# Optimization experiments

Measured on AMD Instinct MI355X. Metric: run time of the kernel, lower is better.

Reference implementation:

```python
import jax, jax.numpy as jnp
import numpy as np

B, S, D = 32, 576, 768
G = 24  # sqrt(S)
TEMP = 0.01


def grid_sample_bilinear_zeros(img, grid):
    # img: (B,C,H,W), grid: (B,Hg,Wg,2) in [-1,1]; torch F.grid_sample,
    # mode='bilinear', padding_mode='zeros', align_corners=False
    Bn, C, H, W = img.shape
    gx, gy = grid[..., 0], grid[..., 1]
    ix = ((gx + 1.0) * W - 1.0) * 0.5
    iy = ((gy + 1.0) * H - 1.0) * 0.5
    x0 = jnp.floor(ix); y0 = jnp.floor(iy)
    x1 = x0 + 1.0;      y1 = y0 + 1.0
    wx1 = ix - x0; wx0 = 1.0 - wx1
    wy1 = iy - y0; wy0 = 1.0 - wy1

    def gather(xi, yi):
        valid = (xi >= 0) & (xi <= W - 1) & (yi >= 0) & (yi <= H - 1)
        xc = jnp.clip(xi, 0, W - 1).astype(jnp.int32)
        yc = jnp.clip(yi, 0, H - 1).astype(jnp.int32)
        vals = jax.vmap(lambda im, y, x: im[:, y, x])(img, yc, xc)  # (B,C,Hg,Wg)
        return vals * valid.astype(img.dtype)[:, None, :, :]

    return (gather(x0, y0) * (wx0 * wy0)[:, None]
            + gather(x1, y0) * (wx1 * wy0)[:, None]
            + gather(x0, y1) * (wx0 * wy1)[:, None]
            + gather(x1, y1) * (wx1 * wy1)[:, None])


def key_finder_net(h, W1, b1, W2, b2, W3, b3):
    # fc1 -> relu -> fc2 -> relu -> fc3 -> tanh
    h = jax.nn.relu(h @ W1 + b1)
    h = jax.nn.relu(h @ W2 + b2)
    return jnp.tanh(h @ W3 + b3)


def setup_inputs() -> dict:
    key = jax.random.key(0)
    ks = jax.random.split(key, 16)
    sd = 1.0 / np.sqrt(D)
    inp = {
        'x': jax.random.normal(ks[0], (B, S, D), dtype=jnp.float32),
        'indices': jax.random.randint(ks[1], (B, S), 0, S),
        'Wq': jax.random.normal(ks[2], (D, D), dtype=jnp.float32) * sd,
        'bq': jnp.zeros((D,), jnp.float32),
        'Wk': jax.random.normal(ks[3], (D, D), dtype=jnp.float32) * sd,
        'bk': jnp.zeros((D,), jnp.float32),
        'Wv': jax.random.normal(ks[4], (D, D), dtype=jnp.float32) * sd,
        'bv': jnp.zeros((D,), jnp.float32),
        'W1': jax.random.normal(ks[5], (2 * D, 60), dtype=jnp.float32) / np.sqrt(2 * D),
        'b1': jnp.zeros((60,), jnp.float32),
        'W2': jax.random.normal(ks[6], (60, 60), dtype=jnp.float32) / np.sqrt(60),
        'b2': jnp.zeros((60,), jnp.float32),
        'W3': jax.random.normal(ks[7], (60, 2), dtype=jnp.float32) / np.sqrt(60),
        'b3': jnp.zeros((2,), jnp.float32),
    }
    return inp


def reference(x, indices, Wq, bq, Wk, bk, Wv, bv, W1, b1, W2, b2, W3, b3):
    q = x @ Wq + bq  # (B,S,D)
    k = x @ Wk + bk
    v = x @ Wv + bv

    sample = key_finder_net(jnp.concatenate([q, k], axis=2), W1, b1, W2, b2, W3, b3)  # (B,S,2)
    # torch: cat((sample_x, sample_y), dim=1).reshape(B,G,G,2)
    flat = jnp.concatenate([sample[:, :, 0], sample[:, :, 1]], axis=1)  # (B,2S)
    grid = flat.reshape(B, G, G, 2)

    k_img = jnp.transpose(k, (0, 2, 1)).reshape(B, D, G, G)
    v_img = jnp.transpose(v, (0, 2, 1)).reshape(B, D, G, G)

    sk = grid_sample_bilinear_zeros(k_img, grid)  # (B,D,G,G)
    sv = grid_sample_bilinear_zeros(v_img, grid)
    sampled_key = jnp.transpose(sk.reshape(B, D, G * G), (0, 2, 1))   # (B,S,D)
    sampled_value = jnp.transpose(sv.reshape(B, D, G * G), (0, 2, 1))

    scores = jnp.sum(q * sampled_key, axis=-1)  # (B,S)
    return jax.nn.sigmoid(TEMP * scores)[..., None] * sampled_value
```

## Files before the change

### kernel.cpp

```cpp
#include <hip/hip_runtime.h>

typedef _Float16 f16;
typedef _Float16 f16x8 __attribute__((ext_vector_type(8)));
typedef _Float16 f16x4 __attribute__((ext_vector_type(4)));
typedef float f32x4 __attribute__((ext_vector_type(4)));

constexpr int NB = 32, NS = 576, ND = 768, NG = 24;
constexpr int M_TOT = NB * NS;
constexpr int N_TOT = 3 * ND;

__global__ void cast_x_kernel(const float* __restrict__ x, f16* __restrict__ xb) {
  int i = (blockIdx.x * 256 + threadIdx.x) * 4;
  float4 v = *(const float4*)(x + i);
  f16x4 o;
  o.x = (f16)v.x; o.y = (f16)v.y; o.z = (f16)v.z; o.w = (f16)v.w;
  *(f16x4*)(xb + i) = o;
}

__global__ __launch_bounds__(256) void cast_w_t_kernel(const float* __restrict__ Wq,
                                                       const float* __restrict__ Wk,
                                                       const float* __restrict__ Wv,
                                                       f16* __restrict__ WT) {
  __shared__ float tile[64][65];
  int bt = blockIdx.x;
  int ntile = bt / 12, ktile = bt % 12;
  const float* src = (ntile < 12) ? Wq : ((ntile < 24) ? Wk : Wv);
  int n0 = (ntile % 12) * 64, k0 = ktile * 64;
  int cc = threadIdx.x & 63, rr = threadIdx.x >> 6;
#pragma unroll
  for (int i = 0; i < 16; i++) {
    int k = rr + i * 4;
    tile[cc][k] = src[(size_t)(k0 + k) * ND + n0 + cc];
  }
  __syncthreads();
#pragma unroll
  for (int i = 0; i < 16; i++) {
    int n = rr + i * 4;
    WT[(size_t)(ntile * 64 + n) * ND + k0 + cc] = (f16)tile[n][cc];
  }
}

__global__ __launch_bounds__(256) void wcT_kernel(const float* __restrict__ Wq,
                                                  const float* __restrict__ Wk,
                                                  const float* __restrict__ bq,
                                                  const float* __restrict__ bk,
                                                  const float* __restrict__ W1,
                                                  const float* __restrict__ b1,
                                                  f16* __restrict__ WcT_hi,
                                                  f16* __restrict__ WcT_lo,
                                                  float* __restrict__ bc) {
  if (blockIdx.x == 768) {
    int c = threadIdx.x;
    if (c < 60) {
      float acc = b1[c];
      for (int j = 0; j < ND; j++)
        acc += bq[j] * W1[j * 60 + c] + bk[j] * W1[(ND + j) * 60 + c];
      bc[c] = acc;
    }
    return;
  }
  __shared__ float part[4][64];
  int r = blockIdx.x;
  int wave = threadIdx.x >> 6, lane = threadIdx.x & 63;
  int c = (lane < 60) ? lane : 59;
  const float* wq = Wq + (size_t)r * ND;
  const float* wk = Wk + (size_t)r * ND;
  float acc = 0.f;
  int j0 = wave * 192;
  for (int j = j0; j < j0 + 192; j++)
    acc += wq[j] * W1[j * 60 + c] + wk[j] * W1[(ND + j) * 60 + c];
  part[wave][lane] = acc;
  __syncthreads();
  if (wave == 0 && lane < 60) {
    float v = part[0][lane] + part[1][lane] + part[2][lane] + part[3][lane];
    f16 hi = (f16)v;
    WcT_hi[(size_t)lane * ND + r] = hi;
    WcT_lo[(size_t)lane * ND + r] = (f16)(v - (float)hi);
  }
}

__device__ __forceinline__ void async_copy16(const f16* g, f16* l) {
  __builtin_amdgcn_global_load_lds((const __attribute__((address_space(1))) void*)g,
                                   (__attribute__((address_space(3))) void*)l, 16, 0, 0);
}

__global__ __launch_bounds__(256) void gemm_kernel(const f16* __restrict__ A,
                                                   const f16* __restrict__ Bt,
                                                   const float* __restrict__ bq,
                                                   const float* __restrict__ bk,
                                                   const float* __restrict__ bv,
                                                   f16* __restrict__ C) {
  constexpr int BM = 128, BK = 64;
  __shared__ __align__(16) f16 sA[BM * BK];
  __shared__ __align__(16) f16 sB[BM * BK];

  int bm = blockIdx.x % (M_TOT / BM);
  int bn = blockIdx.x / (M_TOT / BM);
  int tid = threadIdx.x;
  int wave = tid >> 6, lane = tid & 63;
  int wm = (wave >> 1) * 64, wn = (wave & 1) * 64;
  int m0 = bm * BM, n0 = bn * BM;

  int srow = tid >> 3;
  int gchunk = ((tid & 7) ^ (srow & 7)) * 8;

  f32x4 acc[4][4];
#pragma unroll
  for (int i = 0; i < 4; i++)
#pragma unroll
    for (int j = 0; j < 4; j++) acc[i][j] = 0.f;

  int q = lane >> 4, r16 = lane & 15;

  for (int kk = 0; kk < ND; kk += BK) {
#pragma unroll
    for (int ps = 0; ps < 4; ps++) {
      async_copy16(A + (size_t)(m0 + ps * 32 + srow) * ND + kk + gchunk, sA + ps * 2048 + tid * 8);
      async_copy16(Bt + (size_t)(n0 + ps * 32 + srow) * ND + kk + gchunk, sB + ps * 2048 + tid * 8);
    }
    __syncthreads();

#pragma unroll
    for (int h = 0; h < 2; h++) {
      f16x8 aF[4], bF[4];
#pragma unroll
      for (int mt = 0; mt < 4; mt++) {
        int R = wm + mt * 16 + r16;
        aF[mt] = *(const f16x8*)(sA + R * 64 + (((h * 4 + q) ^ (R & 7)) * 8));
      }
#pragma unroll
      for (int nt = 0; nt < 4; nt++) {
        int R = wn + nt * 16 + r16;
        bF[nt] = *(const f16x8*)(sB + R * 64 + (((h * 4 + q) ^ (R & 7)) * 8));
      }
#pragma unroll
      for (int mt = 0; mt < 4; mt++)
#pragma unroll
        for (int nt = 0; nt < 4; nt++)
          acc[mt][nt] = __builtin_amdgcn_mfma_f32_16x16x32_f16(bF[nt], aF[mt], acc[mt][nt], 0, 0, 0);
    }
    __syncthreads();
  }

#pragma unroll
  for (int mt = 0; mt < 4; mt++) {
    int gm = m0 + wm + mt * 16 + r16;
#pragma unroll
    for (int nt = 0; nt < 4; nt++) {
      int gn0 = n0 + wn + nt * 16 + q * 4;
      const float* bp = (gn0 < ND) ? (bq + gn0)
                      : ((gn0 < 2 * ND) ? (bk + gn0 - ND) : (bv + gn0 - 2 * ND));
      float4 bias = *(const float4*)bp;
      f16x4 o;
      o[0] = (f16)(acc[mt][nt][0] + bias.x);
      o[1] = (f16)(acc[mt][nt][1] + bias.y);
      o[2] = (f16)(acc[mt][nt][2] + bias.z);
      o[3] = (f16)(acc[mt][nt][3] + bias.w);
      *(f16x4*)(C + (size_t)gm * N_TOT + gn0) = o;
    }
  }
}

__global__ __launch_bounds__(256) void z1_mfma_kernel(const float* __restrict__ x,
                                                      const f16* __restrict__ WcT_hi,
                                                      const f16* __restrict__ WcT_lo,
                                                      const float* __restrict__ bc,
                                                      float* __restrict__ h1) {
  __shared__ float red[3][16][64];
  int wave = threadIdx.x >> 6, lane = threadIdx.x & 63;
  int q = lane >> 4, r16 = lane & 15;
  int m0 = blockIdx.x * 16;
  int k0 = wave * 192;
  const float* xr = x + (size_t)(m0 + r16) * ND + k0;

  f32x4 acc[4];
#pragma unroll
  for (int nf = 0; nf < 4; nf++) acc[nf] = 0.f;

  for (int kk = 0; kk < 192; kk += 32) {
    int ko = kk + q * 8;
    float4 v0 = *(const float4*)(xr + ko);
    float4 v1 = *(const float4*)(xr + ko + 4);
    f16x8 a_hi, a_lo;
    float xv[8] = {v0.x, v0.y, v0.z, v0.w, v1.x, v1.y, v1.z, v1.w};
#pragma unroll
    for (int j = 0; j < 8; j++) {
      f16 h = (f16)xv[j];
      a_hi[j] = h;
      a_lo[j] = (f16)(xv[j] - (float)h);
    }
    f16x8 b_hi[4], b_lo[4];
#pragma unroll
    for (int nf = 0; nf < 4; nf++) {
      size_t off = (size_t)(nf * 16 + r16) * ND + k0 + ko;
      b_hi[nf] = *(const f16x8*)(WcT_hi + off);
      b_lo[nf] = *(const f16x8*)(WcT_lo + off);
    }
#pragma unroll
    for (int nf = 0; nf < 4; nf++) {
      acc[nf] = __builtin_amdgcn_mfma_f32_16x16x32_f16(a_hi, b_hi[nf], acc[nf], 0, 0, 0);
      acc[nf] = __builtin_amdgcn_mfma_f32_16x16x32_f16(a_lo, b_hi[nf], acc[nf], 0, 0, 0);
      acc[nf] = __builtin_amdgcn_mfma_f32_16x16x32_f16(a_hi, b_lo[nf], acc[nf], 0, 0, 0);
    }
  }

  if (wave > 0) {
#pragma unroll
    for (int nf = 0; nf < 4; nf++)
#pragma unroll
      for (int r = 0; r < 4; r++) red[wave - 1][nf * 4 + r][lane] = acc[nf][r];
  }
  __syncthreads();
  if (wave == 0) {
#pragma unroll
    for (int nf = 0; nf < 4; nf++) {
      int col = nf * 16 + r16;
      if (col < 60) {
        float bcv = bc[col];
#pragma unroll
        for (int r = 0; r < 4; r++) {
          float v = acc[nf][r] + red[0][nf * 4 + r][lane] + red[1][nf * 4 + r][lane]
                  + red[2][nf * 4 + r][lane] + bcv;
          h1[(size_t)(m0 + q * 4 + r) * 60 + col] = fmaxf(v, 0.f);
        }
      }
    }
  }
}

__global__ void mlp_tail_kernel(const float* __restrict__ h1, const float* __restrict__ W2,
                                const float* __restrict__ b2, const float* __restrict__ W3,
                                const float* __restrict__ b3, float* __restrict__ coords) {
  int m = (blockIdx.x * 256 + threadIdx.x) >> 6;
  int lane = threadIdx.x & 63;
  int cl = (lane < 60) ? lane : 59;
  const float* h = h1 + (size_t)m * 60;
  float acc = b2[cl];
  for (int j = 0; j < 60; j++) acc = fmaf(h[j], W2[j * 60 + cl], acc);
  float h2 = fmaxf(acc, 0.f);
  float p0 = (lane < 60) ? h2 * W3[cl * 2 + 0] : 0.f;
  float p1 = (lane < 60) ? h2 * W3[cl * 2 + 1] : 0.f;
#pragma unroll
  for (int o = 32; o > 0; o >>= 1) { p0 += __shfl_down(p0, o); p1 += __shfl_down(p1, o); }
  if (lane == 0) {
    float s0 = tanhf(p0 + b3[0]);
    float s1 = tanhf(p1 + b3[1]);
    int b = m / NS, s = m % NS;
    float* cb = coords + (size_t)b * (2 * NS);
    cb[(s >> 1) * 2 + (s & 1)] = s0;
    cb[(288 + (s >> 1)) * 2 + (s & 1)] = s1;
  }
}

__global__ __launch_bounds__(256) void sample_kernel(const f16* __restrict__ qkv,
                                                     const float* __restrict__ coords,
                                                     float* __restrict__ out) {
  int wave = threadIdx.x >> 6, t = threadIdx.x & 63;
  int idx = blockIdx.x * 4 + wave;
  int b = idx / NS, p = idx % NS;

  float gx = coords[(size_t)b * (2 * NS) + p * 2 + 0];
  float gy = coords[(size_t)b * (2 * NS) + p * 2 + 1];
  float ix = ((gx + 1.f) * (float)NG - 1.f) * 0.5f;
  float iy = ((gy + 1.f) * (float)NG - 1.f) * 0.5f;
  float x0f = floorf(ix), y0f = floorf(iy);
  float wx1 = ix - x0f, wx0 = 1.f - wx1;
  float wy1 = iy - y0f, wy0 = 1.f - wy1;
  int x0 = (int)x0f, y0 = (int)y0f, x1 = x0 + 1, y1 = y0 + 1;
  bool vx0 = (x0 >= 0) & (x0 <= NG - 1), vx1 = (x1 >= 0) & (x1 <= NG - 1);
  bool vy0 = (y0 >= 0) & (y0 <= NG - 1), vy1 = (y1 >= 0) & (y1 <= NG - 1);
  int cx0 = min(max(x0, 0), NG - 1), cx1 = min(max(x1, 0), NG - 1);
  int cy0 = min(max(y0, 0), NG - 1), cy1 = min(max(y1, 0), NG - 1);
  float w00 = wx0 * wy0 * ((vx0 && vy0) ? 1.f : 0.f);
  float w10 = wx1 * wy0 * ((vx1 && vy0) ? 1.f : 0.f);
  float w01 = wx0 * wy1 * ((vx0 && vy1) ? 1.f : 0.f);
  float w11 = wx1 * wy1 * ((vx1 && vy1) ? 1.f : 0.f);

  size_t base = (size_t)b * NS;
  const f16* r00 = qkv + (base + cy0 * NG + cx0) * N_TOT;
  const f16* r10 = qkv + (base + cy0 * NG + cx1) * N_TOT;
  const f16* r01 = qkv + (base + cy1 * NG + cx0) * N_TOT;
  const f16* r11 = qkv + (base + cy1 * NG + cx1) * N_TOT;
  const f16* qr  = qkv + (base + p) * N_TOT;

  int d0 = t * 12;
  float partial = 0.f;
  float outv[12];
#pragma unroll
  for (int ch = 0; ch < 3; ch++) {
    int d = d0 + ch * 4;
    f16x4 k00 = *(const f16x4*)(r00 + ND + d);
    f16x4 k10 = *(const f16x4*)(r10 + ND + d);
    f16x4 k01 = *(const f16x4*)(r01 + ND + d);
    f16x4 k11 = *(const f16x4*)(r11 + ND + d);
    f16x4 v00 = *(const f16x4*)(r00 + 2 * ND + d);
    f16x4 v10 = *(const f16x4*)(r10 + 2 * ND + d);
    f16x4 v01 = *(const f16x4*)(r01 + 2 * ND + d);
    f16x4 v11 = *(const f16x4*)(r11 + 2 * ND + d);
    f16x4 qv  = *(const f16x4*)(qr + d);
#pragma unroll
    for (int j = 0; j < 4; j++) {
      float sk = w00 * (float)k00[j] + w10 * (float)k10[j]
               + w01 * (float)k01[j] + w11 * (float)k11[j];
      float sv = w00 * (float)v00[j] + w10 * (float)v10[j]
               + w01 * (float)v01[j] + w11 * (float)v11[j];
      partial = fmaf((float)qv[j], sk, partial);
      outv[ch * 4 + j] = sv;
    }
  }
#pragma unroll
  for (int o = 32; o > 0; o >>= 1) partial += __shfl_down(partial, o);
  float score = __shfl(partial, 0);
  float sig = 1.f / (1.f + expf(-0.01f * score));
  float* orow = out + (size_t)(base + p) * ND;
#pragma unroll
  for (int ch = 0; ch < 3; ch++) {
    float4 st;
    st.x = sig * outv[ch * 4 + 0]; st.y = sig * outv[ch * 4 + 1];
    st.z = sig * outv[ch * 4 + 2]; st.w = sig * outv[ch * 4 + 3];
    *(float4*)(orow + d0 + ch * 4) = st;
  }
}

extern "C" void kernel_launch(void* const* d_in, const int* in_sizes, int n_in,
                              void* d_out, int out_size, void* d_ws, size_t ws_size,
                              hipStream_t stream) {
  const float* x  = (const float*)d_in[0];
  const float* Wq = (const float*)d_in[2];
  const float* bq = (const float*)d_in[3];
  const float* Wk = (const float*)d_in[4];
  const float* bk = (const float*)d_in[5];
  const float* Wv = (const float*)d_in[6];
  const float* bv = (const float*)d_in[7];
  const float* W1 = (const float*)d_in[8];
  const float* b1 = (const float*)d_in[9];
  const float* W2 = (const float*)d_in[10];
  const float* b2 = (const float*)d_in[11];
  const float* W3 = (const float*)d_in[12];
  const float* b3 = (const float*)d_in[13];
  float* out = (float*)d_out;

  char* ws = (char*)d_ws;
  f16*   xb     = (f16*)(ws);
  f16*   WT     = (f16*)(ws + 28311552);
  f16*   qkv    = (f16*)(ws + 31850496);
  f16*   WcT_hi = (f16*)(ws + 31850496);
  f16*   WcT_lo = (f16*)(ws + 31948800);
  float* bc     = (float*)(ws + 116969472);
  float* h1     = (float*)(ws + 116969728);
  float* coords = (float*)(ws + 121393408);

  cast_x_kernel<<<dim3(M_TOT * ND / 1024), dim3(256), 0, stream>>>(x, xb);
  cast_w_t_kernel<<<dim3(432), dim3(256), 0, stream>>>(Wq, Wk, Wv, WT);
  wcT_kernel<<<dim3(769), dim3(256), 0, stream>>>(Wq, Wk, bq, bk, W1, b1, WcT_hi, WcT_lo, bc);
  z1_mfma_kernel<<<dim3(M_TOT / 16), dim3(256), 0, stream>>>(x, WcT_hi, WcT_lo, bc, h1);
  gemm_kernel<<<dim3((M_TOT / 128) * (N_TOT / 128)), dim3(256), 0, stream>>>(xb, WT, bq, bk, bv, qkv);
  mlp_tail_kernel<<<dim3(M_TOT / 4), dim3(256), 0, stream>>>(h1, W2, b2, W3, b3, coords);
  sample_kernel<<<dim3(M_TOT / 4), dim3(256), 0, stream>>>(qkv, coords, out);
  (void)in_sizes; (void)n_in; (void)out_size; (void)ws_size;
}
```

Baseline: 355.6 us.

## Fuse x cast and MLP tail into the first-layer MFMA kernel

```diff
diff --git a/kernel.cpp b/kernel.cpp
--- a/kernel.cpp
+++ b/kernel.cpp
@@ -8,14 +8,6 @@
 constexpr int NB = 32, NS = 576, ND = 768, NG = 24;
 constexpr int M_TOT = NB * NS;
 constexpr int N_TOT = 3 * ND;
-
-__global__ void cast_x_kernel(const float* __restrict__ x, f16* __restrict__ xb) {
-  int i = (blockIdx.x * 256 + threadIdx.x) * 4;
-  float4 v = *(const float4*)(x + i);
-  f16x4 o;
-  o.x = (f16)v.x; o.y = (f16)v.y; o.z = (f16)v.z; o.w = (f16)v.w;
-  *(f16x4*)(xb + i) = o;
-}
 
 __global__ __launch_bounds__(256) void cast_w_t_kernel(const float* __restrict__ Wq,
                                                        const float* __restrict__ Wk,
@@ -79,6 +71,106 @@
   }
 }
 
+__global__ __launch_bounds__(256) void z1_fused_kernel(const float* __restrict__ x,
+                                                       const f16* __restrict__ WcT_hi,
+                                                       const f16* __restrict__ WcT_lo,
+                                                       const float* __restrict__ bc,
+                                                       const float* __restrict__ W2,
+                                                       const float* __restrict__ b2,
+                                                       const float* __restrict__ W3,
+                                                       const float* __restrict__ b3,
+                                                       f16* __restrict__ xb,
+                                                       float* __restrict__ coords) {
+  __shared__ float red[3][16][64];
+  __shared__ float htile[16][60];
+  int wave = threadIdx.x >> 6, lane = threadIdx.x & 63;
+  int q = lane >> 4, r16 = lane & 15;
+  int m0 = blockIdx.x * 16;
+  int k0 = wave * 192;
+  const float* xr = x + (size_t)(m0 + r16) * ND + k0;
+  f16* xbr = xb + (size_t)(m0 + r16) * ND + k0;
+
+  f32x4 acc[4];
+#pragma unroll
+  for (int nf = 0; nf < 4; nf++) acc[nf] = 0.f;
+
+  for (int kk = 0; kk < 192; kk += 32) {
+    int ko = kk + q * 8;
+    float4 v0 = *(const float4*)(xr + ko);
+    float4 v1 = *(const float4*)(xr + ko + 4);
+    f16x8 a_hi, a_lo;
+    float xv[8] = {v0.x, v0.y, v0.z, v0.w, v1.x, v1.y, v1.z, v1.w};
+#pragma unroll
+    for (int j = 0; j < 8; j++) {
+      f16 h = (f16)xv[j];
+      a_hi[j] = h;
+      a_lo[j] = (f16)(xv[j] - (float)h);
+    }
+    *(f16x8*)(xbr + ko) = a_hi;
+    f16x8 b_hi[4], b_lo[4];
+#pragma unroll
+    for (int nf = 0; nf < 4; nf++) {
+      size_t off = (size_t)(nf * 16 + r16) * ND + k0 + ko;
+      b_hi[nf] = *(const f16x8*)(WcT_hi + off);
+      b_lo[nf] = *(const f16x8*)(WcT_lo + off);
+    }
+#pragma unroll
+    for (int nf = 0; nf < 4; nf++) {
+      acc[nf] = __builtin_amdgcn_mfma_f32_16x16x32_f16(a_hi, b_hi[nf], acc[nf], 0, 0, 0);
+      acc[nf] = __builtin_amdgcn_mfma_f32_16x16x32_f16(a_lo, b_hi[nf], acc[nf], 0, 0, 0);
+      acc[nf] = __builtin_amdgcn_mfma_f32_16x16x32_f16(a_hi, b_lo[nf], acc[nf], 0, 0, 0);
+    }
+  }
+
+  if (wave > 0) {
+#pragma unroll
+    for (int nf = 0; nf < 4; nf++)
+#pragma unroll
+      for (int r = 0; r < 4; r++) red[wave - 1][nf * 4 + r][lane] = acc[nf][r];
+  }
+  __syncthreads();
+  if (wave == 0) {
+#pragma unroll
+    for (int nf = 0; nf < 4; nf++) {
+      int col = nf * 16 + r16;
+      if (col < 60) {
+        float bcv = bc[col];
+#pragma unroll
+        for (int r = 0; r < 4; r++) {
+          float v = acc[nf][r] + red[0][nf * 4 + r][lane] + red[1][nf * 4 + r][lane]
+                  + red[2][nf * 4 + r][lane] + bcv;
+          htile[q * 4 + r][col] = fmaxf(v, 0.f);
+        }
+      }
+    }
+  }
+  __syncthreads();
+
+  int c = (lane < 60) ? lane : 59;
+  float b2v = b2[c];
+  float w30 = W3[c * 2 + 0], w31 = W3[c * 2 + 1];
+#pragma unroll
+  for (int rr = 0; rr < 4; rr++) {
+    int row = wave * 4 + rr;
+    float acc2 = b2v;
+    for (int j = 0; j < 60; j++) acc2 = fmaf(htile[row][j], W2[j * 60 + c], acc2);
+    float h2 = fmaxf(acc2, 0.f);
+    float p0 = (lane < 60) ? h2 * w30 : 0.f;
+    float p1 = (lane < 60) ? h2 * w31 : 0.f;
+#pragma unroll
+    for (int o = 32; o > 0; o >>= 1) { p0 += __shfl_down(p0, o); p1 += __shfl_down(p1, o); }
+    if (lane == 0) {
+      float s0 = tanhf(p0 + b3[0]);
+      float s1 = tanhf(p1 + b3[1]);
+      int m = m0 + row;
+      int b = m / NS, s = m % NS;
+      float* cb = coords + (size_t)b * (2 * NS);
+      cb[(s >> 1) * 2 + (s & 1)] = s0;
+      cb[(288 + (s >> 1)) * 2 + (s & 1)] = s1;
+    }
+  }
+}
+
 __device__ __forceinline__ void async_copy16(const f16* g, f16* l) {
   __builtin_amdgcn_global_load_lds((const __attribute__((address_space(1))) void*)g,
                                    (__attribute__((address_space(3))) void*)l, 16, 0, 0);
@@ -158,97 +250,6 @@
       o[3] = (f16)(acc[mt][nt][3] + bias.w);
       *(f16x4*)(C + (size_t)gm * N_TOT + gn0) = o;
     }
-  }
-}
-
-__global__ __launch_bounds__(256) void z1_mfma_kernel(const float* __restrict__ x,
-                                                      const f16* __restrict__ WcT_hi,
-                                                      const f16* __restrict__ WcT_lo,
-                                                      const float* __restrict__ bc,
-                                                      float* __restrict__ h1) {
-  __shared__ float red[3][16][64];
-  int wave = threadIdx.x >> 6, lane = threadIdx.x & 63;
-  int q = lane >> 4, r16 = lane & 15;
-  int m0 = blockIdx.x * 16;
-  int k0 = wave * 192;
-  const float* xr = x + (size_t)(m0 + r16) * ND + k0;
-
-  f32x4 acc[4];
-#pragma unroll
-  for (int nf = 0; nf < 4; nf++) acc[nf] = 0.f;
-
-  for (int kk = 0; kk < 192; kk += 32) {
-    int ko = kk + q * 8;
-    float4 v0 = *(const float4*)(xr + ko);
-    float4 v1 = *(const float4*)(xr + ko + 4);
-    f16x8 a_hi, a_lo;
-    float xv[8] = {v0.x, v0.y, v0.z, v0.w, v1.x, v1.y, v1.z, v1.w};
-#pragma unroll
-    for (int j = 0; j < 8; j++) {
-      f16 h = (f16)xv[j];
-      a_hi[j] = h;
-      a_lo[j] = (f16)(xv[j] - (float)h);
-    }
-    f16x8 b_hi[4], b_lo[4];
-#pragma unroll
-    for (int nf = 0; nf < 4; nf++) {
-      size_t off = (size_t)(nf * 16 + r16) * ND + k0 + ko;
-      b_hi[nf] = *(const f16x8*)(WcT_hi + off);
-      b_lo[nf] = *(const f16x8*)(WcT_lo + off);
-    }
-#pragma unroll
-    for (int nf = 0; nf < 4; nf++) {
-      acc[nf] = __builtin_amdgcn_mfma_f32_16x16x32_f16(a_hi, b_hi[nf], acc[nf], 0, 0, 0);
-      acc[nf] = __builtin_amdgcn_mfma_f32_16x16x32_f16(a_lo, b_hi[nf], acc[nf], 0, 0, 0);
-      acc[nf] = __builtin_amdgcn_mfma_f32_16x16x32_f16(a_hi, b_lo[nf], acc[nf], 0, 0, 0);
-    }
-  }
-
-  if (wave > 0) {
-#pragma unroll
-    for (int nf = 0; nf < 4; nf++)
-#pragma unroll
-      for (int r = 0; r < 4; r++) red[wave - 1][nf * 4 + r][lane] = acc[nf][r];
-  }
-  __syncthreads();
-  if (wave == 0) {
-#pragma unroll
-    for (int nf = 0; nf < 4; nf++) {
-      int col = nf * 16 + r16;
-      if (col < 60) {
-        float bcv = bc[col];
-#pragma unroll
-        for (int r = 0; r < 4; r++) {
-          float v = acc[nf][r] + red[0][nf * 4 + r][lane] + red[1][nf * 4 + r][lane]
-                  + red[2][nf * 4 + r][lane] + bcv;
-          h1[(size_t)(m0 + q * 4 + r) * 60 + col] = fmaxf(v, 0.f);
-        }
-      }
-    }
-  }
-}
-
-__global__ void mlp_tail_kernel(const float* __restrict__ h1, const float* __restrict__ W2,
-                                const float* __restrict__ b2, const float* __restrict__ W3,
-                                const float* __restrict__ b3, float* __restrict__ coords) {
-  int m = (blockIdx.x * 256 + threadIdx.x) >> 6;
-  int lane = threadIdx.x & 63;
-  int cl = (lane < 60) ? lane : 59;
-  const float* h = h1 + (size_t)m * 60;
-  float acc = b2[cl];
-  for (int j = 0; j < 60; j++) acc = fmaf(h[j], W2[j * 60 + cl], acc);
-  float h2 = fmaxf(acc, 0.f);
-  float p0 = (lane < 60) ? h2 * W3[cl * 2 + 0] : 0.f;
-  float p1 = (lane < 60) ? h2 * W3[cl * 2 + 1] : 0.f;
-#pragma unroll
-  for (int o = 32; o > 0; o >>= 1) { p0 += __shfl_down(p0, o); p1 += __shfl_down(p1, o); }
-  if (lane == 0) {
-    float s0 = tanhf(p0 + b3[0]);
-    float s1 = tanhf(p1 + b3[1]);
-    int b = m / NS, s = m % NS;
-    float* cb = coords + (size_t)b * (2 * NS);
-    cb[(s >> 1) * 2 + (s & 1)] = s0;
-    cb[(288 + (s >> 1)) * 2 + (s & 1)] = s1;
   }
 }
 
@@ -347,15 +348,13 @@
   f16*   WcT_hi = (f16*)(ws + 31850496);
   f16*   WcT_lo = (f16*)(ws + 31948800);
   float* bc     = (float*)(ws + 116969472);
-  float* h1     = (float*)(ws + 116969728);
   float* coords = (float*)(ws + 121393408);
 
-  cast_x_kernel<<<dim3(M_TOT * ND / 1024), dim3(256), 0, stream>>>(x, xb);
   cast_w_t_kernel<<<dim3(432), dim3(256), 0, stream>>>(Wq, Wk, Wv, WT);
   wcT_kernel<<<dim3(769), dim3(256), 0, stream>>>(Wq, Wk, bq, bk, W1, b1, WcT_hi, WcT_lo, bc);
-  z1_mfma_kernel<<<dim3(M_TOT / 16), dim3(256), 0, stream>>>(x, WcT_hi, WcT_lo, bc, h1);
+  z1_fused_kernel<<<dim3(M_TOT / 16), dim3(256), 0, stream>>>(x, WcT_hi, WcT_lo, bc,
+                                                              W2, b2, W3, b3, xb, coords);
   gemm_kernel<<<dim3((M_TOT / 128) * (N_TOT / 128)), dim3(256), 0, stream>>>(xb, WT, bq, bk, bv, qkv);
-  mlp_tail_kernel<<<dim3(M_TOT / 4), dim3(256), 0, stream>>>(h1, W2, b2, W3, b3, coords);
   sample_kernel<<<dim3(M_TOT / 4), dim3(256), 0, stream>>>(qkv, coords, out);
   (void)in_sizes; (void)n_in; (void)out_size; (void)ws_size;
 }
```

Result: no change. 349.5 us (-1.7%).
